# Kernel tuning notes

Measured on AMD Instinct MI355X. Metric: run time of the kernel, lower is better.

Reference implementation:

```python
import jax, jax.numpy as jnp
import numpy as np


def setup_inputs() -> dict:
    key = jax.random.key(0)
    k1, k2 = jax.random.split(key, 2)
    N, H, W, FIN = 64, 64, 64, 64
    FH, FW, FOUT = 4, 4, 128
    L = (H // FH) * (W // FW)  # 256 output locations (stride == kernel)
    X = jax.random.normal(k1, (N, H, W, FIN), dtype=jnp.float32)
    # 'alexnet' init: normal(0, 0.01), unshared per-location filters
    filters = 0.01 * jax.random.normal(k2, (1, L, FH, FW, FIN, FOUT), dtype=jnp.float32)
    bias = jnp.zeros((FOUT,), dtype=jnp.float32)  # bias init value 0.0
    return {"X": X, "filters": filters, "bias": bias}


def reference(X, filters, bias):
    N, H, W, C = X.shape
    _, L, fh, fw, fin, fout = filters.shape
    rows, cols = H // fh, W // fw
    # image_to_patches (stride==kernel branch): non-overlapping patch extraction
    # patches[n, r*cols+c, i, j, ch] = X[n, r*fh+i, c*fw+j, ch]
    patches = X.reshape(N, rows, fh, cols, fw, C)
    patches = patches.transpose(0, 1, 3, 2, 4, 5).reshape(N, L, fh, fw, C)
    # broadcast-multiply + reduce_sum over (fh, fw, fin) == per-location GEMM
    Z = jnp.einsum('nlijc,lijcf->nlf', patches, filters[0]) + bias
    Z = Z.reshape(N, rows, cols, fout)
    return jax.nn.relu(Z)
```

## Files before the change

kernel.cpp:

```cpp
#include <hip/hip_runtime.h>


typedef __bf16 bf16x8 __attribute__((ext_vector_type(8)));
typedef float f32x4 __attribute__((ext_vector_type(4)));

#define SA 72
#define SBQ 36

__device__ __forceinline__ unsigned pack2(float a, float b) {
  __bf16 lo = (__bf16)a, hi = (__bf16)b;
  unsigned short ul = __builtin_bit_cast(unsigned short, lo);
  unsigned short uh = __builtin_bit_cast(unsigned short, hi);
  return (unsigned)ul | ((unsigned)uh << 16);
}

__global__ __launch_bounds__(256) void bioconv_mfma(
    const float* __restrict__ X, const float* __restrict__ Fw,
    const float* __restrict__ bias, float* __restrict__ out) {
  const int bx = blockIdx.x;
  const int l = bx & 255;
  const int fq = bx >> 8;
  const int r = l >> 4;
  const int c = l & 15;
  const int t = threadIdx.x;
  const int w = t >> 6;
  const int lane = t & 63;
  const int q = lane >> 4;
  const int nl = lane & 15;

  __shared__ __align__(16) unsigned short As[2][64 * SA];
  __shared__ __align__(16) unsigned Bs[2][32 * SBQ];

  const float* Fl = Fw + (size_t)l * 131072 + fq * 32;

  f32x4 acc[2];
  acc[0] = (f32x4){0.f, 0.f, 0.f, 0.f};
  acc[1] = (f32x4){0.f, 0.f, 0.f, 0.f};

  float4 areg[4], b0reg, b1reg;

  const int a_n0 = t >> 4;
  const int a_f4 = t & 15;
  const int b_kp = t >> 3;
  const int b_fo = (t & 7) << 2;

  const float* xrowbase = X + c * 256 + a_f4 * 4;

  auto issue_loads = [&](int s) {
    const int i = s >> 2;
    const int koff = (s & 3) << 6;
    const float* xb = xrowbase + (r * 4 + i) * 4096 + koff;
#pragma unroll
    for (int rep = 0; rep < 4; ++rep) {
      const int n = a_n0 + (rep << 4);
      areg[rep] = *(const float4*)(xb + (size_t)n * 262144);
    }
    const float* g = Fl + s * 8192 + b_kp * 256 + b_fo;
    b0reg = *(const float4*)(g);
    b1reg = *(const float4*)(g + 128);
  };

  auto store_lds = [&](int buf) {
#pragma unroll
    for (int rep = 0; rep < 4; ++rep) {
      const int n = a_n0 + (rep << 4);
      uint2 v;
      v.x = pack2(areg[rep].x, areg[rep].y);
      v.y = pack2(areg[rep].z, areg[rep].w);
      *(uint2*)&As[buf][n * SA + a_f4 * 4] = v;
    }
    uint4 v;
    v.x = pack2(b0reg.x, b1reg.x);
    v.y = pack2(b0reg.y, b1reg.y);
    v.z = pack2(b0reg.z, b1reg.z);
    v.w = pack2(b0reg.w, b1reg.w);
    *(uint4*)&Bs[buf][b_kp * SBQ + b_fo] = v;
  };

  issue_loads(0);
  store_lds(0);

  for (int s = 0; s < 16; ++s) {
    __syncthreads();
    if (s < 15) issue_loads(s + 1);
    const int buf = s & 1;
#pragma unroll
    for (int kc = 0; kc < 2; ++kc) {
      bf16x8 af = *(const bf16x8*)&As[buf][(w * 16 + nl) * SA + kc * 32 + q * 8];
#pragma unroll
      for (int fb = 0; fb < 2; ++fb) {
        const unsigned* bp = &Bs[buf][(kc * 16 + q * 4) * SBQ + fb * 16 + nl];
        uint4 v;
        v.x = bp[0];
        v.y = bp[SBQ];
        v.z = bp[2 * SBQ];
        v.w = bp[3 * SBQ];
        bf16x8 bfr = __builtin_bit_cast(bf16x8, v);
        acc[fb] = __builtin_amdgcn_mfma_f32_16x16x32_bf16(af, bfr, acc[fb], 0, 0, 0);
      }
    }
    if (s < 15) store_lds((s + 1) & 1);
  }

#pragma unroll
  for (int fb = 0; fb < 2; ++fb) {
    const int f = fq * 32 + fb * 16 + nl;
    const float bv = bias[f];
    float* ob = out + (size_t)l * 128 + f;
#pragma unroll
    for (int v = 0; v < 4; ++v) {
      const int n = w * 16 + q * 4 + v;
      const float val = acc[fb][v] + bv;
      ob[(size_t)n * 32768] = fmaxf(val, 0.f);
    }
  }
}

extern "C" void kernel_launch(void* const* d_in, const int* in_sizes, int n_in,
                              void* d_out, int out_size, void* d_ws, size_t ws_size,
                              hipStream_t stream) {
  const float* X = (const float*)d_in[0];
  const float* Fw = (const float*)d_in[1];
  const float* bias = (const float*)d_in[2];
  float* out = (float*)d_out;
  bioconv_mfma<<<1024, 256, 0, stream>>>(X, Fw, bias, out);
}
```

Before: 244.9 us.

## Restructure to single-wave blocks with register-resident A and deeper B prefetch

Each block becomes one 64-lane wave that computes a full 64x32 output tile with four M sub-blocks. The A fragments are loaded straight from global memory into registers in MFMA layout and converted there, so the A LDS staging is gone. Only the filter tile still goes through LDS, with a three-deep register ring for prefetch and no __syncthreads, since a single wave needs no block barrier. The aim is to cut barrier and LDS overhead and keep more filter loads in flight. The cost is more registers and fewer waves per CU to hide memory latency.

```diff
diff --git a/kernel.cpp b/kernel.cpp
--- a/kernel.cpp
+++ b/kernel.cpp
@@ -4,102 +4,113 @@
 typedef __bf16 bf16x8 __attribute__((ext_vector_type(8)));
 typedef float f32x4 __attribute__((ext_vector_type(4)));
 
-#define SA 72
 #define SBQ 36
 
 __device__ __forceinline__ unsigned pack2(float a, float b) {
   __bf16 lo = (__bf16)a, hi = (__bf16)b;
-  unsigned short ul = __builtin_bit_cast(unsigned short, lo);
-  unsigned short uh = __builtin_bit_cast(unsigned short, hi);
-  return (unsigned)ul | ((unsigned)uh << 16);
+  return (unsigned)__builtin_bit_cast(unsigned short, lo) |
+         ((unsigned)__builtin_bit_cast(unsigned short, hi) << 16);
+}
+__device__ __forceinline__ bf16x8 cvt8(float4 lo, float4 hi) {
+  uint4 v;
+  v.x = pack2(lo.x, lo.y);
+  v.y = pack2(lo.z, lo.w);
+  v.z = pack2(hi.x, hi.y);
+  v.w = pack2(hi.z, hi.w);
+  return __builtin_bit_cast(bf16x8, v);
 }
 
-__global__ __launch_bounds__(256) void bioconv_mfma(
+__global__ __launch_bounds__(64) void bioconv_wave(
     const float* __restrict__ X, const float* __restrict__ Fw,
     const float* __restrict__ bias, float* __restrict__ out) {
   const int bx = blockIdx.x;
   const int l = bx & 255;
   const int fq = bx >> 8;
-  const int r = l >> 4;
-  const int c = l & 15;
-  const int t = threadIdx.x;
-  const int w = t >> 6;
-  const int lane = t & 63;
-  const int q = lane >> 4;
-  const int nl = lane & 15;
+  const int r = l >> 4, c = l & 15;
+  const int lane = threadIdx.x;
+  const int q = lane >> 4, nl = lane & 15;
 
-  __shared__ __align__(16) unsigned short As[2][64 * SA];
-  __shared__ __align__(16) unsigned Bs[2][32 * SBQ];
+  __shared__ __align__(16) unsigned Bs[2][16 * SBQ];
 
-  const float* Fl = Fw + (size_t)l * 131072 + fq * 32;
+  const float* pA[4];
+#pragma unroll
+  for (int mb = 0; mb < 4; ++mb)
+    pA[mb] = X + (size_t)(mb * 16 + nl) * 262144 + r * 16384 + c * 256 + q * 8;
 
-  f32x4 acc[2];
-  acc[0] = (f32x4){0.f, 0.f, 0.f, 0.f};
-  acc[1] = (f32x4){0.f, 0.f, 0.f, 0.f};
+  const float* pB = Fw + (size_t)l * 131072 + fq * 32 + (lane >> 3) * 256 + (lane & 7) * 4;
+  unsigned* const wpB = (unsigned*)Bs + ((lane >> 3) * SBQ + (lane & 7) * 4);
 
-  float4 areg[4], b0reg, b1reg;
+  float4 aR[2][8];
+  float4 bR[3][4];
+  f32x4 acc[4][2];
+#pragma unroll
+  for (int mb = 0; mb < 4; ++mb) {
+    acc[mb][0] = (f32x4){0.f, 0.f, 0.f, 0.f};
+    acc[mb][1] = (f32x4){0.f, 0.f, 0.f, 0.f};
+  }
 
-  const int a_n0 = t >> 4;
-  const int a_f4 = t & 15;
-  const int b_kp = t >> 3;
-  const int b_fo = (t & 7) << 2;
-
-  const float* xrowbase = X + c * 256 + a_f4 * 4;
-
-  auto issue_loads = [&](int s) {
-    const int i = s >> 2;
-    const int koff = (s & 3) << 6;
-    const float* xb = xrowbase + (r * 4 + i) * 4096 + koff;
+  auto issueA = [&](int s, int ring) {
+    const int p = s >> 1;
+    const int off = (p >> 2) * 4096 + (p & 3) * 64 + (s & 1) * 32;
 #pragma unroll
-    for (int rep = 0; rep < 4; ++rep) {
-      const int n = a_n0 + (rep << 4);
-      areg[rep] = *(const float4*)(xb + (size_t)n * 262144);
+    for (int mb = 0; mb < 4; ++mb) {
+      aR[ring][mb * 2] = *(const float4*)(pA[mb] + off);
+      aR[ring][mb * 2 + 1] = *(const float4*)(pA[mb] + off + 4);
     }
-    const float* g = Fl + s * 8192 + b_kp * 256 + b_fo;
-    b0reg = *(const float4*)(g);
-    b1reg = *(const float4*)(g + 128);
+  };
+  auto issueB = [&](int s, int ring) {
+#pragma unroll
+    for (int rep = 0; rep < 2; ++rep) {
+      const float* g = pB + s * 4096 + rep * 2048;
+      bR[ring][rep * 2] = *(const float4*)(g);
+      bR[ring][rep * 2 + 1] = *(const float4*)(g + 128);
+    }
+  };
+  auto writeB = [&](int s, int ring) {
+    unsigned* wp = wpB + (s & 1) * (16 * SBQ);
+#pragma unroll
+    for (int rep = 0; rep < 2; ++rep) {
+      float4 e0 = bR[ring][rep * 2], e1 = bR[ring][rep * 2 + 1];
+      uint4 v;
+      v.x = pack2(e0.x, e1.x);
+      v.y = pack2(e0.y, e1.y);
+      v.z = pack2(e0.z, e1.z);
+      v.w = pack2(e0.w, e1.w);
+      *(uint4*)(wp + rep * 8 * SBQ) = v;
+    }
   };
 
-  auto store_lds = [&](int buf) {
+  issueA(0, 0);
+  issueB(0, 0);
+  issueA(1, 1);
+  issueB(1, 1);
+  issueB(2, 2);
+  writeB(0, 0);
+
 #pragma unroll
-    for (int rep = 0; rep < 4; ++rep) {
-      const int n = a_n0 + (rep << 4);
-      uint2 v;
-      v.x = pack2(areg[rep].x, areg[rep].y);
-      v.y = pack2(areg[rep].z, areg[rep].w);
-      *(uint2*)&As[buf][n * SA + a_f4 * 4] = v;
+  for (int s = 0; s < 32; ++s) {
+    if (s + 3 < 32) issueB(s + 3, (s + 3) % 3);
+    if (s + 1 < 32) writeB(s + 1, (s + 1) % 3);
+
+    bf16x8 af[4];
+#pragma unroll
+    for (int mb = 0; mb < 4; ++mb)
+      af[mb] = cvt8(aR[s & 1][mb * 2], aR[s & 1][mb * 2 + 1]);
+    if (s + 2 < 32) issueA(s + 2, s & 1);
+
+#pragma unroll
+    for (int fb = 0; fb < 2; ++fb) {
+      const unsigned* bp = &Bs[s & 1][(q * 4) * SBQ + fb * 16 + nl];
+      uint4 v;
+      v.x = bp[0];
+      v.y = bp[SBQ];
+      v.z = bp[2 * SBQ];
+      v.w = bp[3 * SBQ];
+      bf16x8 bfr = __builtin_bit_cast(bf16x8, v);
+#pragma unroll
+      for (int mb = 0; mb < 4; ++mb)
+        acc[mb][fb] = __builtin_amdgcn_mfma_f32_16x16x32_bf16(af[mb], bfr, acc[mb][fb], 0, 0, 0);
     }
-    uint4 v;
-    v.x = pack2(b0reg.x, b1reg.x);
-    v.y = pack2(b0reg.y, b1reg.y);
-    v.z = pack2(b0reg.z, b1reg.z);
-    v.w = pack2(b0reg.w, b1reg.w);
-    *(uint4*)&Bs[buf][b_kp * SBQ + b_fo] = v;
-  };
-
-  issue_loads(0);
-  store_lds(0);
-
-  for (int s = 0; s < 16; ++s) {
-    __syncthreads();
-    if (s < 15) issue_loads(s + 1);
-    const int buf = s & 1;
-#pragma unroll
-    for (int kc = 0; kc < 2; ++kc) {
-      bf16x8 af = *(const bf16x8*)&As[buf][(w * 16 + nl) * SA + kc * 32 + q * 8];
-#pragma unroll
-      for (int fb = 0; fb < 2; ++fb) {
-        const unsigned* bp = &Bs[buf][(kc * 16 + q * 4) * SBQ + fb * 16 + nl];
-        uint4 v;
-        v.x = bp[0];
-        v.y = bp[SBQ];
-        v.z = bp[2 * SBQ];
-        v.w = bp[3 * SBQ];
-        bf16x8 bfr = __builtin_bit_cast(bf16x8, v);
-        acc[fb] = __builtin_amdgcn_mfma_f32_16x16x32_bf16(af, bfr, acc[fb], 0, 0, 0);
-      }
-    }
-    if (s < 15) store_lds((s + 1) & 1);
   }
 
 #pragma unroll
@@ -108,10 +119,12 @@
     const float bv = bias[f];
     float* ob = out + (size_t)l * 128 + f;
 #pragma unroll
-    for (int v = 0; v < 4; ++v) {
-      const int n = w * 16 + q * 4 + v;
-      const float val = acc[fb][v] + bv;
-      ob[(size_t)n * 32768] = fmaxf(val, 0.f);
+    for (int mb = 0; mb < 4; ++mb) {
+#pragma unroll
+      for (int v = 0; v < 4; ++v) {
+        const int row = mb * 16 + q * 4 + v;
+        ob[(size_t)row * 32768] = fmaxf(acc[mb][fb][v] + bv, 0.f);
+      }
     }
   }
 }
@@ -123,5 +136,5 @@
   const float* Fw = (const float*)d_in[1];
   const float* bias = (const float*)d_in[2];
   float* out = (float*)d_out;
-  bioconv_mfma<<<1024, 256, 0, stream>>>(X, Fw, bias, out);
+  bioconv_wave<<<1024, 64, 0, stream>>>(X, Fw, bias, out);
 }
```

Measured after the change: 240.1 us. 2.0% less time.

## Stream filters via async global-to-LDS loads and read X directly into registers

Applied to the files above, without the earlier changes.

The filters now go straight from global memory into LDS with global_load_lds, double-buffered across 512-thread blocks that each cover 64 output channels, so half as many blocks are launched. X patches are loaded directly into registers and converted to bf16 per wave, skipping LDS staging for A. The goal is less register staging and conversion work and fewer redundant X reads across channel blocks. In exchange, each B element is now packed from fp32 in LDS at read time, the stride-65 LDS reads are scalar, and there is no explicit wait on the async LDS loads, which makes correctness depend on the barrier alone.

```diff
diff --git a/kernel.cpp b/kernel.cpp
--- a/kernel.cpp
+++ b/kernel.cpp
@@ -4,114 +4,107 @@
 typedef __bf16 bf16x8 __attribute__((ext_vector_type(8)));
 typedef float f32x4 __attribute__((ext_vector_type(4)));
 
-#define SA 72
-#define SBQ 36
+#define SB 65
 
 __device__ __forceinline__ unsigned pack2(float a, float b) {
   __bf16 lo = (__bf16)a, hi = (__bf16)b;
-  unsigned short ul = __builtin_bit_cast(unsigned short, lo);
-  unsigned short uh = __builtin_bit_cast(unsigned short, hi);
-  return (unsigned)ul | ((unsigned)uh << 16);
+  return (unsigned)__builtin_bit_cast(unsigned short, lo) |
+         ((unsigned)__builtin_bit_cast(unsigned short, hi) << 16);
+}
+__device__ __forceinline__ bf16x8 cvt8(float4 lo, float4 hi) {
+  uint4 v;
+  v.x = pack2(lo.x, lo.y);
+  v.y = pack2(lo.z, lo.w);
+  v.z = pack2(hi.x, hi.y);
+  v.w = pack2(hi.z, hi.w);
+  return __builtin_bit_cast(bf16x8, v);
+}
+__device__ __forceinline__ void gl_lds4(const float* g, float* lds) {
+  __builtin_amdgcn_global_load_lds(
+      (const __attribute__((address_space(1))) void*)g,
+      (__attribute__((address_space(3))) void*)lds, 4, 0, 0);
 }
 
-__global__ __launch_bounds__(256) void bioconv_mfma(
+__global__ __launch_bounds__(512, 4) void bioconv_async(
     const float* __restrict__ X, const float* __restrict__ Fw,
     const float* __restrict__ bias, float* __restrict__ out) {
   const int bx = blockIdx.x;
   const int l = bx & 255;
-  const int fq = bx >> 8;
-  const int r = l >> 4;
-  const int c = l & 15;
+  const int fh = bx >> 8;
+  const int r = l >> 4, c = l & 15;
   const int t = threadIdx.x;
   const int w = t >> 6;
+  const int wf = w & 3;
+  const int wn = w >> 2;
   const int lane = t & 63;
-  const int q = lane >> 4;
-  const int nl = lane & 15;
+  const int q = lane >> 4, nl = lane & 15;
 
-  __shared__ __align__(16) unsigned short As[2][64 * SA];
-  __shared__ __align__(16) unsigned Bs[2][32 * SBQ];
+  __shared__ __align__(16) float Bs[2][64 * SB];
 
-  const float* Fl = Fw + (size_t)l * 131072 + fq * 32;
+  const float* pA[2];
+#pragma unroll
+  for (int mb = 0; mb < 2; ++mb)
+    pA[mb] = X + (size_t)(wn * 32 + mb * 16 + nl) * 262144 + r * 16384 + c * 256 + q * 8;
+
+  const int kw = w * 8;
+  const float* pB = Fw + (size_t)l * 131072 + fh * 64 + (size_t)kw * 128 + lane;
 
   f32x4 acc[2];
   acc[0] = (f32x4){0.f, 0.f, 0.f, 0.f};
   acc[1] = (f32x4){0.f, 0.f, 0.f, 0.f};
 
-  float4 areg[4], b0reg, b1reg;
-
-  const int a_n0 = t >> 4;
-  const int a_f4 = t & 15;
-  const int b_kp = t >> 3;
-  const int b_fo = (t & 7) << 2;
-
-  const float* xrowbase = X + c * 256 + a_f4 * 4;
-
-  auto issue_loads = [&](int s) {
-    const int i = s >> 2;
-    const int koff = (s & 3) << 6;
-    const float* xb = xrowbase + (r * 4 + i) * 4096 + koff;
+  auto issueB = [&](int s, int buf) {
+    const float* g = pB + (size_t)s * 8192;
+    float* ldsrow = &Bs[buf][kw * SB];
 #pragma unroll
-    for (int rep = 0; rep < 4; ++rep) {
-      const int n = a_n0 + (rep << 4);
-      areg[rep] = *(const float4*)(xb + (size_t)n * 262144);
-    }
-    const float* g = Fl + s * 8192 + b_kp * 256 + b_fo;
-    b0reg = *(const float4*)(g);
-    b1reg = *(const float4*)(g + 128);
+    for (int i = 0; i < 8; ++i)
+      gl_lds4(g + i * 128, ldsrow + i * SB);
   };
 
-  auto store_lds = [&](int buf) {
-#pragma unroll
-    for (int rep = 0; rep < 4; ++rep) {
-      const int n = a_n0 + (rep << 4);
-      uint2 v;
-      v.x = pack2(areg[rep].x, areg[rep].y);
-      v.y = pack2(areg[rep].z, areg[rep].w);
-      *(uint2*)&As[buf][n * SA + a_f4 * 4] = v;
-    }
-    uint4 v;
-    v.x = pack2(b0reg.x, b1reg.x);
-    v.y = pack2(b0reg.y, b1reg.y);
-    v.z = pack2(b0reg.z, b1reg.z);
-    v.w = pack2(b0reg.w, b1reg.w);
-    *(uint4*)&Bs[buf][b_kp * SBQ + b_fo] = v;
-  };
-
-  issue_loads(0);
-  store_lds(0);
+  issueB(0, 0);
+  __syncthreads();
 
   for (int s = 0; s < 16; ++s) {
-    __syncthreads();
-    if (s < 15) issue_loads(s + 1);
+    if (s + 1 < 16) issueB(s + 1, (s + 1) & 1);
+
+    const int pixoff = (s >> 2) * 4096 + (s & 3) * 64;
+    bf16x8 af[2][2];
+#pragma unroll
+    for (int mb = 0; mb < 2; ++mb) {
+      float4 lo0 = *(const float4*)(pA[mb] + pixoff);
+      float4 hi0 = *(const float4*)(pA[mb] + pixoff + 4);
+      float4 lo1 = *(const float4*)(pA[mb] + pixoff + 32);
+      float4 hi1 = *(const float4*)(pA[mb] + pixoff + 36);
+      af[0][mb] = cvt8(lo0, hi0);
+      af[1][mb] = cvt8(lo1, hi1);
+    }
+
     const int buf = s & 1;
 #pragma unroll
     for (int kc = 0; kc < 2; ++kc) {
-      bf16x8 af = *(const bf16x8*)&As[buf][(w * 16 + nl) * SA + kc * 32 + q * 8];
-#pragma unroll
-      for (int fb = 0; fb < 2; ++fb) {
-        const unsigned* bp = &Bs[buf][(kc * 16 + q * 4) * SBQ + fb * 16 + nl];
-        uint4 v;
-        v.x = bp[0];
-        v.y = bp[SBQ];
-        v.z = bp[2 * SBQ];
-        v.w = bp[3 * SBQ];
-        bf16x8 bfr = __builtin_bit_cast(bf16x8, v);
-        acc[fb] = __builtin_amdgcn_mfma_f32_16x16x32_bf16(af, bfr, acc[fb], 0, 0, 0);
-      }
+      const float* bp = &Bs[buf][(kc * 32 + q * 8) * SB + wf * 16 + nl];
+      uint4 bw;
+      bw.x = pack2(bp[0], bp[SB]);
+      bw.y = pack2(bp[2 * SB], bp[3 * SB]);
+      bw.z = pack2(bp[4 * SB], bp[5 * SB]);
+      bw.w = pack2(bp[6 * SB], bp[7 * SB]);
+      bf16x8 bfr = __builtin_bit_cast(bf16x8, bw);
+      acc[0] = __builtin_amdgcn_mfma_f32_16x16x32_bf16(af[kc][0], bfr, acc[0], 0, 0, 0);
+      acc[1] = __builtin_amdgcn_mfma_f32_16x16x32_bf16(af[kc][1], bfr, acc[1], 0, 0, 0);
     }
-    if (s < 15) store_lds((s + 1) & 1);
+
+    __syncthreads();
   }
 
+  const int f = fh * 64 + wf * 16 + nl;
+  const float bv = bias[f];
+  float* ob = out + (size_t)l * 128 + f;
 #pragma unroll
-  for (int fb = 0; fb < 2; ++fb) {
-    const int f = fq * 32 + fb * 16 + nl;
-    const float bv = bias[f];
-    float* ob = out + (size_t)l * 128 + f;
+  for (int mb = 0; mb < 2; ++mb) {
 #pragma unroll
     for (int v = 0; v < 4; ++v) {
-      const int n = w * 16 + q * 4 + v;
-      const float val = acc[fb][v] + bv;
-      ob[(size_t)n * 32768] = fmaxf(val, 0.f);
+      const int row = wn * 32 + mb * 16 + q * 4 + v;
+      ob[(size_t)row * 32768] = fmaxf(acc[mb][v] + bv, 0.f);
     }
   }
 }
@@ -123,5 +116,5 @@
   const float* Fw = (const float*)d_in[1];
   const float* bias = (const float*)d_in[2];
   float* out = (float*)d_out;
-  bioconv_mfma<<<1024, 256, 0, stream>>>(X, Fw, bias, out);
+  bioconv_async<<<512, 512, 0, stream>>>(X, Fw, bias, out);
 }
```

After: 246.7 us. Within noise of the previous version (+0.7%).
